# Kernel tuning notes

Measured on AMD Instinct MI355X. Metric: run time of the kernel, lower is better.

## Reference

```python
import jax, jax.numpy as jnp
import numpy as np

B, S, D = 2, 2048, 2048
HQ, HKV, HD, HDV = 32, 8, 64, 64
QPK = HQ // HKV
EPS = 1e-5


def setup_inputs() -> dict:
    key = jax.random.key(0)
    ks = jax.random.split(key, 10)
    s = lambda fan_in: 1.0 / np.sqrt(fan_in)
    return {
        'x': jax.random.normal(ks[0], (B, S, D), dtype=jnp.float32),
        'ln_g': jnp.ones((D,), jnp.float32),
        'ln_b': jnp.zeros((D,), jnp.float32),
        'Wq': jax.random.uniform(ks[1], (D, HQ * HD), jnp.float32, -s(D), s(D)),
        'bq': jax.random.uniform(ks[2], (HQ * HD,), jnp.float32, -s(D), s(D)),
        'Wk': jax.random.uniform(ks[3], (D, HKV * HD), jnp.float32, -s(D), s(D)),
        'bk': jax.random.uniform(ks[4], (HKV * HD,), jnp.float32, -s(D), s(D)),
        'Wv': jax.random.uniform(ks[5], (D, HKV * HDV), jnp.float32, -s(D), s(D)),
        'bv': jax.random.uniform(ks[6], (HKV * HDV,), jnp.float32, -s(D), s(D)),
        'Wo': jax.random.uniform(ks[7], (HQ * HDV, D), jnp.float32, -s(HQ * HDV), s(HQ * HDV)),
        'bo': jax.random.uniform(ks[8], (D,), jnp.float32, -s(HQ * HDV), s(HQ * HDV)),
    }


def reference(x, ln_g, ln_b, Wq, bq, Wk, bk, Wv, bv, Wo, bo):
    # LayerNorm
    mu = jnp.mean(x, axis=-1, keepdims=True)
    var = jnp.mean(jnp.square(x - mu), axis=-1, keepdims=True)
    xn = (x - mu) * jax.lax.rsqrt(var + EPS) * ln_g + ln_b

    q = (xn @ Wq + bq).reshape(B, S, HKV, QPK, HD) * (1.0 / np.sqrt(HD))
    k = (xn @ Wk + bk).reshape(B, S, HKV, HD)
    v = (xn @ Wv + bv).reshape(B, S, HKV, HDV)

    # scores: (b, t=query, T=key, h, q_per_kv)
    scores = jnp.einsum('bthqd,bThd->btThq', q, k)
    # causal mask: -inf where T > t (upper triangle above diagonal)
    mask = jnp.triu(jnp.full((S, S), -jnp.inf, dtype=scores.dtype), 1)
    scores = scores + mask[None, :, :, None, None]
    # NOTE: source softmaxes over dim=-4, i.e. the QUERY axis t -> axis=1 here
    scores = jax.nn.softmax(scores, axis=1)
    out = jnp.einsum('btThq,bThd->bthqd', scores, v)
    out = out.reshape(B, S, HQ * HDV)
    return out @ Wo + bo
```

## Files before the change

### kernel.cpp

```cpp
#include <hip/hip_runtime.h>

#define Bb  2
#define Ss  2048
#define Dd  2048
#define HKV 8
#define QPK 4
#define HD  64
#define MR  (Bb * Ss)
#define NQ  2048
#define NKV 512

#define LOG2E 1.4426950408889634f

typedef unsigned short u16;
typedef __attribute__((ext_vector_type(8))) short s16x8;
typedef __attribute__((ext_vector_type(4))) float f32x4;

__device__ __forceinline__ u16 f2bf(float f) {
  unsigned u = __float_as_uint(f);
  u += 0x7fffu + ((u >> 16) & 1u);
  return (u16)(u >> 16);
}

__device__ __forceinline__ void gload16(const u16* g, u16* l) {
  __builtin_amdgcn_global_load_lds(
      (const __attribute__((address_space(1))) unsigned int*)g,
      (__attribute__((address_space(3))) unsigned int*)l, 16, 0, 0);
}

__global__ __launch_bounds__(256) void ln_kernel(
    const float* __restrict__ x, const float* __restrict__ g,
    const float* __restrict__ be, u16* __restrict__ xn)
{
  int row = blockIdx.x;
  int tid = threadIdx.x;
  const float4* xr = (const float4*)(x + (size_t)row * Dd);
  float4 a = xr[tid];
  float4 b4 = xr[tid + 256];
  float s  = a.x + a.y + a.z + a.w + b4.x + b4.y + b4.z + b4.w;
  float ss = a.x*a.x + a.y*a.y + a.z*a.z + a.w*a.w
           + b4.x*b4.x + b4.y*b4.y + b4.z*b4.z + b4.w*b4.w;
  #pragma unroll
  for (int off = 32; off > 0; off >>= 1) {
    s  += __shfl_down(s, off);
    ss += __shfl_down(ss, off);
  }
  __shared__ float red[8];
  int lane = tid & 63, w = tid >> 6;
  if (lane == 0) { red[w] = s; red[4 + w] = ss; }
  __syncthreads();
  s  = red[0] + red[1] + red[2] + red[3];
  ss = red[4] + red[5] + red[6] + red[7];
  float mu = s * (1.0f / Dd);
  float rs = rsqrtf(ss * (1.0f / Dd) - mu * mu + 1e-5f);

  u16* xo = xn + (size_t)row * Dd;
  const float4* gv4 = (const float4*)g;
  const float4* bv4 = (const float4*)be;
  #pragma unroll
  for (int p = 0; p < 2; ++p) {
    int idx = tid + p * 256;
    float4 xv = (p == 0) ? a : b4;
    float4 gg = gv4[idx], bb = bv4[idx];
    ushort4 pk;
    pk.x = f2bf((xv.x - mu) * rs * gg.x + bb.x);
    pk.y = f2bf((xv.y - mu) * rs * gg.y + bb.y);
    pk.z = f2bf((xv.z - mu) * rs * gg.z + bb.z);
    pk.w = f2bf((xv.w - mu) * rs * gg.w + bb.w);
    *(ushort4*)(xo + idx * 4) = pk;
  }
}

__global__ __launch_bounds__(256) void transpose_cast(
    const float* __restrict__ W, u16* __restrict__ WT, int K, int N)
{
  __shared__ float tile[32][33];
  int tx = threadIdx.x & 31, ty = threadIdx.x >> 5;
  int n0 = blockIdx.x * 32, k0 = blockIdx.y * 32;
  #pragma unroll
  for (int i = 0; i < 4; ++i)
    tile[ty + 8 * i][tx] = W[(size_t)(k0 + ty + 8 * i) * N + n0 + tx];
  __syncthreads();
  #pragma unroll
  for (int i = 0; i < 4; ++i)
    WT[(size_t)(n0 + ty + 8 * i) * K + k0 + tx] = f2bf(tile[tx][ty + 8 * i]);
}

__global__ __launch_bounds__(256) void transpose_v(
    const u16* __restrict__ vb, u16* __restrict__ vT)
{
  __shared__ u16 tile[32][33];
  int tx = threadIdx.x & 31, ty = threadIdx.x >> 5;
  int c0 = blockIdx.x * 32;
  int r0 = blockIdx.y * 32;
  #pragma unroll
  for (int i = 0; i < 4; ++i)
    tile[ty + 8 * i][tx] = vb[(size_t)(r0 + ty + 8 * i) * NKV + c0 + tx];
  __syncthreads();
  int b = r0 >> 11, t = r0 & 2047;
  #pragma unroll
  for (int i = 0; i < 4; ++i)
    vT[((size_t)(b * NKV + c0 + ty + 8 * i)) * Ss + t + tx] = tile[tx][ty + 8 * i];
}

__device__ __forceinline__ void gemm_core128(
    const u16* __restrict__ A, const u16* __restrict__ BT, int K,
    int brow128, int bcol128, u16* __restrict__ As, u16* __restrict__ Bs,
    f32x4 (&acc)[4][4])
{
  int tid  = threadIdx.x;
  int lane = tid & 63, wave = tid >> 6;
  int wm = (wave >> 1) * 64, wn = (wave & 1) * 64;
  int m16 = lane & 15, quad = lane >> 4;
  int srow = lane >> 3;
  int scol = (lane & 7) * 8;
  const u16* Ag = A  + (size_t)(brow128 + wave * 32 + srow) * K + scol;
  const u16* Bg = BT + (size_t)(bcol128 + wave * 32 + srow) * K + scol;
  u16* Asw = As + (size_t)(wave * 32) * 64;
  u16* Bsw = Bs + (size_t)(wave * 32) * 64;

  for (int k0 = 0; k0 < K; k0 += 64) {
    __syncthreads();
    #pragma unroll
    for (int i = 0; i < 4; ++i) {
      gload16(Ag + (size_t)(i * 8) * K + k0, Asw + i * 512);
      gload16(Bg + (size_t)(i * 8) * K + k0, Bsw + i * 512);
    }
    __syncthreads();
    s16x8 af[4][2], bf[4][2];
    #pragma unroll
    for (int i = 0; i < 4; ++i) {
      af[i][0] = *(const s16x8*)&As[(size_t)(wm + i * 16 + m16) * 64 + quad * 8];
      af[i][1] = *(const s16x8*)&As[(size_t)(wm + i * 16 + m16) * 64 + 32 + quad * 8];
      bf[i][0] = *(const s16x8*)&Bs[(size_t)(wn + i * 16 + m16) * 64 + quad * 8];
      bf[i][1] = *(const s16x8*)&Bs[(size_t)(wn + i * 16 + m16) * 64 + 32 + quad * 8];
    }
    #pragma unroll
    for (int i = 0; i < 4; ++i)
      #pragma unroll
      for (int j = 0; j < 4; ++j) {
        acc[i][j] = __builtin_amdgcn_mfma_f32_16x16x32_bf16(af[i][0], bf[j][0], acc[i][j], 0, 0, 0);
        acc[i][j] = __builtin_amdgcn_mfma_f32_16x16x32_bf16(af[i][1], bf[j][1], acc[i][j], 0, 0, 0);
      }
  }
}

template<bool BF16OUT>
__global__ __launch_bounds__(256) void gemm_bt2(
    const u16* __restrict__ A, const u16* __restrict__ BT,
    const float* __restrict__ bias, void* __restrict__ Cv,
    int N, int K, float scale)
{
  __shared__ u16 As[128 * 64];
  __shared__ u16 Bs[128 * 64];
  f32x4 acc[4][4] = {};
  gemm_core128(A, BT, K, blockIdx.y * 128, blockIdx.x * 128, As, Bs, acc);

  int lane = threadIdx.x & 63, wave = threadIdx.x >> 6;
  int wm = (wave >> 1) * 64, wn = (wave & 1) * 64;
  int m16 = lane & 15, quad = lane >> 4;
  #pragma unroll
  for (int i = 0; i < 4; ++i) {
    #pragma unroll
    for (int j = 0; j < 4; ++j) {
      int col = blockIdx.x * 128 + wn + j * 16 + m16;
      float bcol = bias[col];
      #pragma unroll
      for (int r = 0; r < 4; ++r) {
        int rowg = blockIdx.y * 128 + wm + i * 16 + quad * 4 + r;
        float val = (acc[i][j][r] + bcol) * scale;
        if constexpr (BF16OUT)
          ((u16*)Cv)[(size_t)rowg * N + col] = f2bf(val);
        else
          ((float*)Cv)[(size_t)rowg * N + col] = val;
      }
    }
  }
}

__global__ __launch_bounds__(256) void gemm_qkv(
    const u16* __restrict__ A, const u16* __restrict__ BT,
    const float* __restrict__ bq, const float* __restrict__ bk,
    const float* __restrict__ bv,
    u16* __restrict__ qb, u16* __restrict__ kb, u16* __restrict__ vb)
{
  __shared__ u16 As[128 * 64];
  __shared__ u16 Bs[128 * 64];
  f32x4 acc[4][4] = {};
  gemm_core128(A, BT, Dd, blockIdx.y * 128, blockIdx.x * 128, As, Bs, acc);

  u16* outp; const float* bp; int ldo, colbase; float scale;
  if (blockIdx.x < 16)      { outp = qb; bp = bq; ldo = NQ;  colbase = blockIdx.x * 128;        scale = 0.125f * LOG2E; }
  else if (blockIdx.x < 20) { outp = kb; bp = bk; ldo = NKV; colbase = (blockIdx.x - 16) * 128; scale = 1.0f; }
  else                      { outp = vb; bp = bv; ldo = NKV; colbase = (blockIdx.x - 20) * 128; scale = 1.0f; }

  int lane = threadIdx.x & 63, wave = threadIdx.x >> 6;
  int wm = (wave >> 1) * 64, wn = (wave & 1) * 64;
  int m16 = lane & 15, quad = lane >> 4;
  #pragma unroll
  for (int i = 0; i < 4; ++i) {
    #pragma unroll
    for (int j = 0; j < 4; ++j) {
      int col = colbase + wn + j * 16 + m16;
      float bcol = bp[col];
      #pragma unroll
      for (int r = 0; r < 4; ++r) {
        int rowg = blockIdx.y * 128 + wm + i * 16 + quad * 4 + r;
        outp[(size_t)rowg * ldo + col] = f2bf((acc[i][j][r] + bcol) * scale);
      }
    }
  }
}

__global__ __launch_bounds__(256) void pass_a_mfma(
    const u16* __restrict__ qb, const u16* __restrict__ kb,
    float* __restrict__ cst)
{
  __shared__ u16 Qs[64][70];
  int combo = blockIdx.x;
  int qk = combo & 3, bh = combo >> 2;
  int b = bh >> 3, h = bh & 7;
  int g = blockIdx.y;
  int tid = threadIdx.x;
  int lane = tid & 63, wave = tid >> 6;
  int m16 = lane & 15, quad = lane >> 4;
  int T0w = g * 128 + wave * 32;

  const u16* kbase = kb + (size_t)b * Ss * NKV + h * HD;
  const u16* qbase = qb + (size_t)b * Ss * NQ + (h * QPK + qk) * HD;

  s16x8 kf[2][2];
  #pragma unroll
  for (int jg = 0; jg < 2; ++jg)
    #pragma unroll
    for (int kh = 0; kh < 2; ++kh)
      kf[jg][kh] = *(const s16x8*)(kbase + (size_t)(T0w + jg * 16 + m16) * NKV + kh * 32 + quad * 8);

  float ms[2] = {-1e30f, -1e30f};
  float ls[2] = {0.f, 0.f};
  int sr = tid >> 3, sc = (tid & 7) * 8;
  int tDiag = T0w & ~63;

  for (int t0 = g * 128; t0 < Ss; t0 += 64) {
    __syncthreads();
    *(int4*)&Qs[sr][sc]      = *(const int4*)(qbase + (size_t)(t0 + sr) * NQ + sc);
    *(int4*)&Qs[sr + 32][sc] = *(const int4*)(qbase + (size_t)(t0 + sr + 32) * NQ + sc);
    __syncthreads();
    if (t0 + 63 < T0w) continue;

    s16x8 af[4][2];
    #pragma unroll
    for (int i = 0; i < 4; ++i) {
      af[i][0] = *(const s16x8*)&Qs[i * 16 + m16][quad * 8];
      af[i][1] = *(const s16x8*)&Qs[i * 16 + m16][32 + quad * 8];
    }
    f32x4 acc[4][2];
    #pragma unroll
    for (int i = 0; i < 4; ++i)
      #pragma unroll
      for (int jg = 0; jg < 2; ++jg) {
        f32x4 z = {};
        z = __builtin_amdgcn_mfma_f32_16x16x32_bf16(af[i][0], kf[jg][0], z, 0, 0, 0);
        acc[i][jg] = __builtin_amdgcn_mfma_f32_16x16x32_bf16(af[i][1], kf[jg][1], z, 0, 0, 0);
      }
    if (t0 == tDiag) {
      #pragma unroll
      for (int i = 0; i < 4; ++i)
        #pragma unroll
        for (int jg = 0; jg < 2; ++jg) {
          int tg = t0 + i * 16 + quad * 4;
          int Tg = T0w + jg * 16 + m16;
          #pragma unroll
          for (int r = 0; r < 4; ++r)
            if (tg + r < Tg) acc[i][jg][r] = -3e38f;
        }
    }
    #pragma unroll
    for (int jg = 0; jg < 2; ++jg) {
      float bm = -3e38f;
      #pragma unroll
      for (int i = 0; i < 4; ++i)
        #pragma unroll
        for (int r = 0; r < 4; ++r) bm = fmaxf(bm, acc[i][jg][r]);
      float mn = fmaxf(ms[jg], bm);
      float se = 0.f;
      #pragma unroll
      for (int i = 0; i < 4; ++i)
        #pragma unroll
        for (int r = 0; r < 4; ++r) se += exp2f(acc[i][jg][r] - mn);
      ls[jg] = ls[jg] * exp2f(ms[jg] - mn) + se;
      ms[jg] = mn;
    }
  }
  #pragma unroll
  for (int jg = 0; jg < 2; ++jg) {
    float m = ms[jg], l = ls[jg];
    #pragma unroll
    for (int off = 16; off <= 32; off <<= 1) {
      float mo = __shfl_xor(m, off);
      float lo = __shfl_xor(l, off);
      float mn = fmaxf(m, mo);
      l = l * exp2f(m - mn) + lo * exp2f(mo - mn);
      m = mn;
    }
    if (quad == 0)
      cst[(size_t)(bh * QPK + qk) * Ss + T0w + jg * 16 + m16] = m + __log2f(l);
  }
}

__global__ __launch_bounds__(256) void pass_b_mfma(
    const u16* __restrict__ qb, const u16* __restrict__ kb,
    const u16* __restrict__ vT, const float* __restrict__ cst,
    u16* __restrict__ attn)
{
  __shared__ u16 Ks[64][70];
  __shared__ u16 Vs[64][70];
  __shared__ u16 P[4][16][70];
  int combo = blockIdx.x;
  int qk = combo & 3, bh = combo >> 2;
  int b = bh >> 3, h = bh & 7;
  int g = 31 - blockIdx.y;
  int tid = threadIdx.x;
  int lane = tid & 63, wave = tid >> 6;
  int m16 = lane & 15, quad = lane >> 4;
  int trow = g * 64 + wave * 16;

  const u16* qbase = qb + (size_t)b * Ss * NQ + (h * QPK + qk) * HD;
  const u16* kbase = kb + (size_t)b * Ss * NKV + h * HD;
  const u16* vbase = vT + (size_t)(bh * 64) * Ss;
  const float* cbase = cst + (size_t)(bh * QPK + qk) * Ss;

  s16x8 qf[2];
  #pragma unroll
  for (int kh = 0; kh < 2; ++kh)
    qf[kh] = *(const s16x8*)(qbase + (size_t)(trow + m16) * NQ + kh * 32 + quad * 8);

  f32x4 oacc[4] = {};
  int sr = tid >> 3, sc = (tid & 7) * 8;
  int Tend = g * 64;

  for (int T0 = 0; T0 <= Tend; T0 += 64) {
    __syncthreads();
    *(int4*)&Ks[sr][sc]      = *(const int4*)(kbase + (size_t)(T0 + sr) * NKV + sc);
    *(int4*)&Ks[sr + 32][sc] = *(const int4*)(kbase + (size_t)(T0 + sr + 32) * NKV + sc);
    *(int4*)&Vs[sr][sc]      = *(const int4*)(vbase + (size_t)sr * Ss + T0 + sc);
    *(int4*)&Vs[sr + 32][sc] = *(const int4*)(vbase + (size_t)(sr + 32) * Ss + T0 + sc);
    __syncthreads();
    bool diag = (T0 == Tend);
    #pragma unroll
    for (int i = 0; i < 4; ++i) {
      s16x8 k0 = *(const s16x8*)&Ks[i * 16 + m16][quad * 8];
      s16x8 k1 = *(const s16x8*)&Ks[i * 16 + m16][32 + quad * 8];
      f32x4 z = {};
      z = __builtin_amdgcn_mfma_f32_16x16x32_bf16(k0, qf[0], z, 0, 0, 0);
      z = __builtin_amdgcn_mfma_f32_16x16x32_bf16(k1, qf[1], z, 0, 0, 0);
      float4 cc = *(const float4*)(cbase + T0 + i * 16 + quad * 4);
      float w0 = exp2f(z[0] - cc.x);
      float w1 = exp2f(z[1] - cc.y);
      float w2 = exp2f(z[2] - cc.z);
      float w3 = exp2f(z[3] - cc.w);
      if (diag) {
        int t  = trow + m16;
        int Tg = T0 + i * 16 + quad * 4;
        if (Tg + 0 > t) w0 = 0.f;
        if (Tg + 1 > t) w1 = 0.f;
        if (Tg + 2 > t) w2 = 0.f;
        if (Tg + 3 > t) w3 = 0.f;
      }
      unsigned u0 = __float_as_uint(w0) + 0x8000u;
      unsigned u1 = __float_as_uint(w1) + 0x8000u;
      unsigned u2 = __float_as_uint(w2) + 0x8000u;
      unsigned u3 = __float_as_uint(w3) + 0x8000u;
      uint2 pk;
      pk.x = (u0 >> 16) | (u1 & 0xffff0000u);
      pk.y = (u2 >> 16) | (u3 & 0xffff0000u);
      *(uint2*)&P[wave][m16][i * 16 + quad * 4] = pk;
    }
    #pragma unroll
    for (int kh = 0; kh < 2; ++kh) {
      s16x8 pa = *(const s16x8*)&P[wave][m16][kh * 32 + quad * 8];
      #pragma unroll
      for (int dj = 0; dj < 4; ++dj) {
        s16x8 vf = *(const s16x8*)&Vs[dj * 16 + m16][kh * 32 + quad * 8];
        oacc[dj] = __builtin_amdgcn_mfma_f32_16x16x32_bf16(pa, vf, oacc[dj], 0, 0, 0);
      }
    }
  }
  u16* abase = attn + (size_t)b * Ss * NQ + (h * QPK + qk) * HD;
  #pragma unroll
  for (int dj = 0; dj < 4; ++dj)
    #pragma unroll
    for (int r = 0; r < 4; ++r)
      abase[(size_t)(trow + quad * 4 + r) * NQ + dj * 16 + m16] = f2bf(oacc[dj][r]);
}

extern "C" void kernel_launch(void* const* d_in, const int* in_sizes, int n_in,
                              void* d_out, int out_size, void* d_ws, size_t ws_size,
                              hipStream_t stream)
{
  (void)in_sizes; (void)n_in; (void)out_size; (void)ws_size;
  const float* x   = (const float*)d_in[0];
  const float* lng = (const float*)d_in[1];
  const float* lnb = (const float*)d_in[2];
  const float* Wq  = (const float*)d_in[3];
  const float* bq  = (const float*)d_in[4];
  const float* Wk  = (const float*)d_in[5];
  const float* bk  = (const float*)d_in[6];
  const float* Wv  = (const float*)d_in[7];
  const float* bv  = (const float*)d_in[8];
  const float* Wo  = (const float*)d_in[9];
  const float* bo  = (const float*)d_in[10];
  float* out = (float*)d_out;

  char* ws = (char*)d_ws;
  size_t off = 0;
  auto take = [&](size_t bytes) -> char* {
    char* p = ws + off;
    off += (bytes + 255) & ~(size_t)255;
    return p;
  };
  u16*    xnb   = (u16*)take((size_t)MR * Dd * 2);
  u16*    wqkvT = (u16*)take((size_t)(NQ + 2 * NKV) * Dd * 2);
  u16*    woT   = (u16*)take((size_t)Dd * NQ * 2);
  u16*    qbB   = (u16*)take((size_t)MR * NQ * 2);
  u16*    kbB   = (u16*)take((size_t)MR * NKV * 2);
  u16*    vbB   = (u16*)take((size_t)MR * NKV * 2);
  u16*    vTb   = (u16*)take((size_t)MR * NKV * 2);
  float*  cst   = (float*)take((size_t)Bb * HKV * QPK * Ss * 4);
  u16*    attnb = (u16*)take((size_t)MR * NQ * 2);

  ln_kernel<<<MR, 256, 0, stream>>>(x, lng, lnb, xnb);
  transpose_cast<<<dim3(NQ / 32, Dd / 32), 256, 0, stream>>>(Wq, wqkvT, Dd, NQ);
  transpose_cast<<<dim3(NKV / 32, Dd / 32), 256, 0, stream>>>(Wk, wqkvT + (size_t)NQ * Dd, Dd, NKV);
  transpose_cast<<<dim3(NKV / 32, Dd / 32), 256, 0, stream>>>(Wv, wqkvT + (size_t)(NQ + NKV) * Dd, Dd, NKV);
  transpose_cast<<<dim3(NQ / 32, Dd / 32), 256, 0, stream>>>(Wo, woT, Dd, NQ);

  gemm_qkv<<<dim3((NQ + 2 * NKV) / 128, MR / 128), 256, 0, stream>>>(
      xnb, wqkvT, bq, bk, bv, qbB, kbB, vbB);
  transpose_v<<<dim3(NKV / 32, MR / 32), 256, 0, stream>>>(vbB, vTb);

  pass_a_mfma<<<dim3(64, 16), 256, 0, stream>>>(qbB, kbB, cst);
  pass_b_mfma<<<dim3(64, 32), 256, 0, stream>>>(qbB, kbB, vTb, cst, attnb);

  gemm_bt2<false><<<dim3(Dd / 128, MR / 128), 256, 0, stream>>>(
      attnb, woT, bo, out, Dd, NQ, 1.0f);
}
```

Before: 432.4 us.

## Use direct-to-LDS loads with XOR swizzle and register-permuted P in attention passes

Replaces register-staged global-to-LDS copies of Q, K and V tiles with global_load_lds into unpadded 64x64 tiles that use an XOR slot swizzle to avoid bank conflicts. In pass B, the P tile no longer round-trips through shared memory. Softmax weights are packed with v_cvt_pk_bf16_f32 and moved into MFMA A-operand layout with permlane32/16 swaps. This removes LDS traffic, barriers-related latency and VGPR staging, at the risk of getting the lane permutation or swizzle mapping wrong.

```diff
diff --git a/kernel.cpp b/kernel.cpp
--- a/kernel.cpp
+++ b/kernel.cpp
@@ -13,6 +13,7 @@
 #define LOG2E 1.4426950408889634f
 
 typedef unsigned short u16;
+typedef unsigned int u32;
 typedef __attribute__((ext_vector_type(8))) short s16x8;
 typedef __attribute__((ext_vector_type(4))) float f32x4;
 
@@ -26,6 +27,12 @@
   __builtin_amdgcn_global_load_lds(
       (const __attribute__((address_space(1))) unsigned int*)g,
       (__attribute__((address_space(3))) unsigned int*)l, 16, 0, 0);
+}
+
+__device__ __forceinline__ u32 cvtpk_bf16(float a, float b) {
+  u32 r;
+  asm volatile("v_cvt_pk_bf16_f32 %0, %1, %2" : "=v"(r) : "v"(a), "v"(b));
+  return r;
 }
 
 __global__ __launch_bounds__(256) void ln_kernel(
@@ -216,7 +223,7 @@
     const u16* __restrict__ qb, const u16* __restrict__ kb,
     float* __restrict__ cst)
 {
-  __shared__ u16 Qs[64][70];
+  __shared__ u16 Qs[64 * 64];
   int combo = blockIdx.x;
   int qk = combo & 3, bh = combo >> 2;
   int b = bh >> 3, h = bh & 7;
@@ -233,26 +240,30 @@
   #pragma unroll
   for (int jg = 0; jg < 2; ++jg)
     #pragma unroll
-    for (int kh = 0; kh < 2; ++kh)
-      kf[jg][kh] = *(const s16x8*)(kbase + (size_t)(T0w + jg * 16 + m16) * NKV + kh * 32 + quad * 8);
+    for (int dc = 0; dc < 2; ++dc)
+      kf[jg][dc] = *(const s16x8*)(kbase + (size_t)(T0w + jg * 16 + m16) * NKV + dc * 32 + quad * 8);
 
   float ms[2] = {-1e30f, -1e30f};
   float ls[2] = {0.f, 0.f};
-  int sr = tid >> 3, sc = (tid & 7) * 8;
+  int srow  = (wave << 3) + (lane >> 3);
+  int slot0 = (lane & 7) ^ (lane >> 3);
+  u16* QsW = Qs + (size_t)(wave * 8) * 64;
+  int sl0 = quad ^ (m16 & 7);
+  int sl1 = (quad | 4) ^ (m16 & 7);
   int tDiag = T0w & ~63;
 
   for (int t0 = g * 128; t0 < Ss; t0 += 64) {
     __syncthreads();
-    *(int4*)&Qs[sr][sc]      = *(const int4*)(qbase + (size_t)(t0 + sr) * NQ + sc);
-    *(int4*)&Qs[sr + 32][sc] = *(const int4*)(qbase + (size_t)(t0 + sr + 32) * NQ + sc);
+    gload16(qbase + (size_t)(t0 + srow) * NQ + slot0 * 8, QsW);
+    gload16(qbase + (size_t)(t0 + srow + 32) * NQ + slot0 * 8, QsW + 32 * 64);
     __syncthreads();
     if (t0 + 63 < T0w) continue;
 
     s16x8 af[4][2];
     #pragma unroll
     for (int i = 0; i < 4; ++i) {
-      af[i][0] = *(const s16x8*)&Qs[i * 16 + m16][quad * 8];
-      af[i][1] = *(const s16x8*)&Qs[i * 16 + m16][32 + quad * 8];
+      af[i][0] = *(const s16x8*)&Qs[(i * 16 + m16) * 64 + sl0 * 8];
+      af[i][1] = *(const s16x8*)&Qs[(i * 16 + m16) * 64 + sl1 * 8];
     }
     f32x4 acc[4][2];
     #pragma unroll
@@ -313,9 +324,8 @@
     const u16* __restrict__ vT, const float* __restrict__ cst,
     u16* __restrict__ attn)
 {
-  __shared__ u16 Ks[64][70];
-  __shared__ u16 Vs[64][70];
-  __shared__ u16 P[4][16][70];
+  __shared__ u16 Ks[64 * 64];
+  __shared__ u16 Vs[64 * 64];
   int combo = blockIdx.x;
   int qk = combo & 3, bh = combo >> 2;
   int b = bh >> 3, h = bh & 7;
@@ -332,56 +342,64 @@
 
   s16x8 qf[2];
   #pragma unroll
-  for (int kh = 0; kh < 2; ++kh)
-    qf[kh] = *(const s16x8*)(qbase + (size_t)(trow + m16) * NQ + kh * 32 + quad * 8);
+  for (int dc = 0; dc < 2; ++dc)
+    qf[dc] = *(const s16x8*)(qbase + (size_t)(trow + m16) * NQ + dc * 32 + quad * 8);
 
   f32x4 oacc[4] = {};
-  int sr = tid >> 3, sc = (tid & 7) * 8;
+  int srow  = (wave << 3) + (lane >> 3);
+  int slot0 = (lane & 7) ^ (lane >> 3);
+  u16* KsW = Ks + (size_t)(wave * 8) * 64;
+  u16* VsW = Vs + (size_t)(wave * 8) * 64;
+  int sl0 = quad ^ (m16 & 7);
+  int sl1 = (quad | 4) ^ (m16 & 7);
   int Tend = g * 64;
 
   for (int T0 = 0; T0 <= Tend; T0 += 64) {
     __syncthreads();
-    *(int4*)&Ks[sr][sc]      = *(const int4*)(kbase + (size_t)(T0 + sr) * NKV + sc);
-    *(int4*)&Ks[sr + 32][sc] = *(const int4*)(kbase + (size_t)(T0 + sr + 32) * NKV + sc);
-    *(int4*)&Vs[sr][sc]      = *(const int4*)(vbase + (size_t)sr * Ss + T0 + sc);
-    *(int4*)&Vs[sr + 32][sc] = *(const int4*)(vbase + (size_t)(sr + 32) * Ss + T0 + sc);
+    gload16(kbase + (size_t)(T0 + srow) * NKV + slot0 * 8, KsW);
+    gload16(kbase + (size_t)(T0 + srow + 32) * NKV + slot0 * 8, KsW + 32 * 64);
+    gload16(vbase + (size_t)srow * Ss + T0 + slot0 * 8, VsW);
+    gload16(vbase + (size_t)(srow + 32) * Ss + T0 + slot0 * 8, VsW + 32 * 64);
     __syncthreads();
     bool diag = (T0 == Tend);
     #pragma unroll
-    for (int i = 0; i < 4; ++i) {
-      s16x8 k0 = *(const s16x8*)&Ks[i * 16 + m16][quad * 8];
-      s16x8 k1 = *(const s16x8*)&Ks[i * 16 + m16][32 + quad * 8];
-      f32x4 z = {};
-      z = __builtin_amdgcn_mfma_f32_16x16x32_bf16(k0, qf[0], z, 0, 0, 0);
-      z = __builtin_amdgcn_mfma_f32_16x16x32_bf16(k1, qf[1], z, 0, 0, 0);
-      float4 cc = *(const float4*)(cbase + T0 + i * 16 + quad * 4);
-      float w0 = exp2f(z[0] - cc.x);
-      float w1 = exp2f(z[1] - cc.y);
-      float w2 = exp2f(z[2] - cc.z);
-      float w3 = exp2f(z[3] - cc.w);
-      if (diag) {
-        int t  = trow + m16;
-        int Tg = T0 + i * 16 + quad * 4;
-        if (Tg + 0 > t) w0 = 0.f;
-        if (Tg + 1 > t) w1 = 0.f;
-        if (Tg + 2 > t) w2 = 0.f;
-        if (Tg + 3 > t) w3 = 0.f;
-      }
-      unsigned u0 = __float_as_uint(w0) + 0x8000u;
-      unsigned u1 = __float_as_uint(w1) + 0x8000u;
-      unsigned u2 = __float_as_uint(w2) + 0x8000u;
-      unsigned u3 = __float_as_uint(w3) + 0x8000u;
-      uint2 pk;
-      pk.x = (u0 >> 16) | (u1 & 0xffff0000u);
-      pk.y = (u2 >> 16) | (u3 & 0xffff0000u);
-      *(uint2*)&P[wave][m16][i * 16 + quad * 4] = pk;
-    }
-    #pragma unroll
-    for (int kh = 0; kh < 2; ++kh) {
-      s16x8 pa = *(const s16x8*)&P[wave][m16][kh * 32 + quad * 8];
+    for (int tc = 0; tc < 2; ++tc) {
+      u32 A[2], Bw[2];
+      #pragma unroll
+      for (int ii = 0; ii < 2; ++ii) {
+        int i = tc * 2 + ii;
+        s16x8 k0 = *(const s16x8*)&Ks[(i * 16 + m16) * 64 + sl0 * 8];
+        s16x8 k1 = *(const s16x8*)&Ks[(i * 16 + m16) * 64 + sl1 * 8];
+        f32x4 z = {};
+        z = __builtin_amdgcn_mfma_f32_16x16x32_bf16(k0, qf[0], z, 0, 0, 0);
+        z = __builtin_amdgcn_mfma_f32_16x16x32_bf16(k1, qf[1], z, 0, 0, 0);
+        float4 cc = *(const float4*)(cbase + T0 + i * 16 + quad * 4);
+        float w0 = exp2f(z[0] - cc.x);
+        float w1 = exp2f(z[1] - cc.y);
+        float w2 = exp2f(z[2] - cc.z);
+        float w3 = exp2f(z[3] - cc.w);
+        if (diag) {
+          int t  = trow + m16;
+          int Tg = T0 + i * 16 + quad * 4;
+          if (Tg + 0 > t) w0 = 0.f;
+          if (Tg + 1 > t) w1 = 0.f;
+          if (Tg + 2 > t) w2 = 0.f;
+          if (Tg + 3 > t) w3 = 0.f;
+        }
+        A[ii]  = cvtpk_bf16(w0, w1);
+        Bw[ii] = cvtpk_bf16(w2, w3);
+      }
+      asm volatile("v_permlane32_swap_b32 %0, %1" : "+v"(A[0]),  "+v"(A[1]));
+      asm volatile("v_permlane16_swap_b32 %0, %1" : "+v"(A[0]),  "+v"(A[1]));
+      asm volatile("v_permlane32_swap_b32 %0, %1" : "+v"(Bw[0]), "+v"(Bw[1]));
+      asm volatile("v_permlane16_swap_b32 %0, %1" : "+v"(Bw[0]), "+v"(Bw[1]));
+      union { uint4 u; s16x8 v; } pu;
+      pu.u.x = A[0]; pu.u.y = Bw[0]; pu.u.z = A[1]; pu.u.w = Bw[1];
+      s16x8 pa = pu.v;
       #pragma unroll
       for (int dj = 0; dj < 4; ++dj) {
-        s16x8 vf = *(const s16x8*)&Vs[dj * 16 + m16][kh * 32 + quad * 8];
+        int vsl = (quad | (tc << 2)) ^ (m16 & 7);
+        s16x8 vf = *(const s16x8*)&Vs[(dj * 16 + m16) * 64 + vsl * 8];
         oacc[dj] = __builtin_amdgcn_mfma_f32_16x16x32_bf16(pa, vf, oacc[dj], 0, 0, 0);
       }
     }
```

Result: faster. 397.8 us (-8.0%).
